# Kernel tuning notes

Hardware: AMD Instinct MI355X
Metric: run time of the kernel (lower is better)

## Reference

```python
import jax, jax.numpy as jnp
import numpy as np

K = 8
EPS = 1e-8


def setup_inputs() -> dict:
    key = jax.random.key(0)
    tokens = jax.random.normal(key, (32, 1024, 256), dtype=jnp.float32)
    return {"tokens": tokens}


def reference(tokens) -> jnp.ndarray:
    # tokens: [B, N, D] -> adjacency [B, N, N] float32 (0/1), mutual kNN, no self-loops
    B, N, D = tokens.shape
    tn = tokens / (jnp.linalg.norm(tokens, axis=-1, keepdims=True) + EPS)
    sim = jnp.einsum('bnd,bmd->bnm', tn, tn)  # [B, N, N] cosine similarity
    # mask diagonal (add_self=False)
    diag = jnp.eye(N, dtype=bool)
    sim = jnp.where(diag[None, :, :], -jnp.inf, sim)
    k = min(K, N - 1)
    _, topk_idx = jax.lax.top_k(sim, k)  # [B, N, k]
    b_idx = jnp.arange(B)[:, None, None]
    r_idx = jnp.arange(N)[None, :, None]
    adj = jnp.zeros((B, N, N), dtype=bool).at[b_idx, r_idx, topk_idx].set(True)
    # mutual kNN: keep edge only if both directions selected
    adj = adj & jnp.swapaxes(adj, 1, 2)
    return adj.astype(jnp.float32)
```

## Files before the change

### kernel.cpp

```cpp
#include <hip/hip_runtime.h>
#include <math.h>
#include <stdint.h>

#define B_ 32
#define N_ 1024
#define D_ 256
#define K_ 8
#define CAND 12

typedef unsigned short u16;
typedef unsigned int u32;
typedef __attribute__((ext_vector_type(8))) short s16x8;
typedef __attribute__((ext_vector_type(16))) float f32x16;

__device__ inline void cp16(const void* g, void* l) {
    __builtin_amdgcn_global_load_lds((const __attribute__((address_space(1))) void*)g,
                                     (__attribute__((address_space(3))) void*)l, 16, 0, 0);
}

__device__ inline u16 f2bf(float f) {
    uint32_t u = __float_as_uint(f);
    return (u16)((u + 0x7fffu + ((u >> 16) & 1u)) >> 16);
}
__device__ inline u32 umax32(u32 a, u32 b) { return a > b ? a : b; }
__device__ inline u32 umin32(u32 a, u32 b) { return a < b ? a : b; }

__global__ __launch_bounds__(256) void prep_kernel(const float* __restrict__ tok,
                                                   double* __restrict__ invn,
                                                   u16* __restrict__ xhi) {
    const int tid = threadIdx.x;
    const int wave = tid >> 6, lane = tid & 63;
    const int row = blockIdx.x * 4 + wave;
    const float4 v = *reinterpret_cast<const float4*>(tok + (size_t)row * D_ + lane * 4);
    double s = (double)v.x * v.x + (double)v.y * v.y +
               (double)v.z * v.z + (double)v.w * v.w;
    #pragma unroll
    for (int off = 32; off > 0; off >>= 1) s += __shfl_xor(s, off, 64);
    const double inv = 1.0 / (sqrt(s) + 1e-8);
    if (lane == 0) invn[row] = inv;
    ushort4 h;
    h.x = f2bf((float)(v.x * inv));
    h.y = f2bf((float)(v.y * inv));
    h.z = f2bf((float)(v.z * inv));
    h.w = f2bf((float)(v.w * inv));
    *reinterpret_cast<ushort4*>(xhi + (size_t)row * D_ + lane * 4) = h;
}

__global__ __launch_bounds__(256, 4) void sim_topk_kernel(const u16* __restrict__ Xhi,
                                                          u32* __restrict__ candk,
                                                          int* __restrict__ candj) {
    __shared__ __align__(16) char smem[16384];
    char* tiles = smem;
    u32*  keysL = (u32*)smem;

    const int id    = blockIdx.x;
    const int chunk = id >> 3;
    const int b   = (id & 7) * 4 + (chunk >> 5);
    const int rem = chunk & 31;
    const int i0  = (rem >> 1) * 64;
    const int jh  = rem & 1;

    const int tid = threadIdx.x;
    const int w = tid >> 6, lane = tid & 63;
    const int mq = w >> 1, nq = w & 1;
    const int half = lane >> 5;
    const int il = lane & 31;

    const u16* XhiB = Xhi + (size_t)b * N_ * D_;

    const int srr = lane >> 3, spp = lane & 7;
    const int sgoff = (spp ^ srr) * 8;
    const int srow  = w * 16 + srr;

    const int ra = mq * 32 + il;
    const int rb = nq * 32 + il;
    const int xa = ra & 7, xb = rb & 7;

    s16x8 Ahf[4][4];
    #pragma unroll
    for (int kc = 0; kc < 4; ++kc) {
        __syncthreads();
        #pragma unroll
        for (int t = 0; t < 2; ++t) {
            const int rr = srow + t * 8;
            cp16(XhiB + (size_t)(i0 + rr) * D_ + kc * 64 + sgoff,
                 tiles + w * 2048 + t * 1024);
        }
        __syncthreads();
        #pragma unroll
        for (int ks = 0; ks < 4; ++ks) {
            const int ca = ((ks * 2 + half) ^ xa) * 16;
            Ahf[kc][ks] = *(const s16x8*)(tiles + ra * 128 + ca);
        }
    }
    __syncthreads();

    auto STAGE_B = [&](int round, int bufn) {
        const int j0n = (jh * 8 + (round >> 2)) * 64;
        const int kcn = round & 3;
        char* bdst = tiles + bufn * 8192 + w * 2048;
        #pragma unroll
        for (int t = 0; t < 2; ++t) {
            const int rr = srow + t * 8;
            cp16(XhiB + (size_t)(j0n + rr) * D_ + kcn * 64 + sgoff, bdst + t * 1024);
        }
    };

    const int diag_jt = i0 >> 6;
    u32 keys[CAND];
    #pragma unroll
    for (int c = 0; c < CAND; ++c) keys[c] = 0u;

    STAGE_B(0, 0);

    for (int lt = 0; lt < 8; ++lt) {
        const int jt = jh * 8 + lt;
        f32x16 acc;
        #pragma unroll
        for (int c = 0; c < 16; ++c) acc[c] = 0.0f;

        #pragma unroll
        for (int kc = 0; kc < 4; ++kc) {
            const int r = lt * 4 + kc;
            const int cur = r & 1;
            if (r < 31) {
                STAGE_B(r + 1, cur ^ 1);
                asm volatile("s_waitcnt vmcnt(2)" ::: "memory");
            } else {
                asm volatile("s_waitcnt vmcnt(0)" ::: "memory");
            }
            __builtin_amdgcn_s_barrier();
            __builtin_amdgcn_sched_barrier(0);
            const char* bb = tiles + cur * 8192;
            #pragma unroll
            for (int ks = 0; ks < 4; ++ks) {
                const int cb = ((ks * 2 + half) ^ xb) * 16;
                const s16x8 bh = *(const s16x8*)(bb + rb * 128 + cb);
                acc = __builtin_amdgcn_mfma_f32_32x32x16_bf16(bh, Ahf[kc][ks], acc, 0, 0, 0);
            }
            __builtin_amdgcn_sched_barrier(0);
            __builtin_amdgcn_s_barrier();
        }

        const u32 codebase = (u32)(jt << 4);
        const bool diag = (jt == diag_jt) && (mq == nq);
        #pragma unroll
        for (int rg = 0; rg < 16; ++rg) {
            const u32 u = __float_as_uint(acc[rg]);
            const u32 mono = u ^ ((u32)(((int)u) >> 31) | 0x80000000u);
            u32 key = (mono & 0xFFFFFF00u) | (codebase + (u32)rg);
            if (diag && ((rg & 3) + 8 * (rg >> 2) + 4 * half == il)) key = 0u;
            u32 t = key;
            #pragma unroll
            for (int c = 0; c < CAND; ++c) {
                const u32 hi = umax32(keys[c], t);
                t = umin32(keys[c], t);
                keys[c] = hi;
            }
        }
    }

    __syncthreads();
    {
        const int r = mq * 32 + il;
        const int s = nq * 2 + half;
        u32* dst = keysL + (r * 4 + s) * CAND;
        #pragma unroll
        for (int c = 0; c < CAND; ++c) dst[c] = keys[c];
    }
    __syncthreads();

    if (tid < 64) {
        const u32* kl = keysL + tid * (4 * CAND);
        const size_t base = ((size_t)(b * N_ + i0 + tid) * 2 + jh) * CAND;
        int p0 = 0, p1 = 0, p2 = 0, p3 = 0;
        #pragma unroll
        for (int o = 0; o < CAND; ++o) {
            const u32 k0v = kl[p0];
            const u32 k1v = kl[CAND + p1];
            const u32 k2v = kl[2 * CAND + p2];
            const u32 k3v = kl[3 * CAND + p3];
            int bg = 0; u32 bv = k0v;
            if (k1v > bv) { bv = k1v; bg = 1; }
            if (k2v > bv) { bv = k2v; bg = 2; }
            if (k3v > bv) { bv = k3v; bg = 3; }
            const int code = (int)(bv & 0xFFu);
            const int jtv = code >> 4, rg = code & 15;
            candk[base + o] = bv;
            candj[base + o] = jtv * 64 + (bg >> 1) * 32 + (rg & 3) + 8 * (rg >> 2)
                              + 4 * (bg & 1);
            p0 += (bg == 0); p1 += (bg == 1); p2 += (bg == 2); p3 += (bg == 3);
        }
    }
}

__global__ __launch_bounds__(512) void merge_rescore_kernel(const u32* __restrict__ candk,
                                                            const int* __restrict__ candj,
                                                            const float* __restrict__ tok,
                                                            const double* __restrict__ invn,
                                                            int* __restrict__ topk) {
    __shared__ int    mj[32 * CAND];
    __shared__ double dv[32 * CAND];
    const int tid = threadIdx.x;

    const int id    = blockIdx.x;
    const int chunk = id >> 3;
    const int b     = (id & 7) * 4 + (chunk >> 5);
    const int i0    = (chunk & 31) * 32;
    const int R0    = b * N_ + i0;

    if (tid < 32) {
        const size_t base = (size_t)(R0 + tid) * 2 * CAND;
        int p0 = 0, p1 = 0;
        #pragma unroll
        for (int o = 0; o < CAND; ++o) {
            const u32 k0 = candk[base + p0];
            const u32 k1 = candk[base + CAND + p1];
            if (k0 >= k1) { mj[tid * CAND + o] = candj[base + p0];        ++p0; }
            else          { mj[tid * CAND + o] = candj[base + CAND + p1]; ++p1; }
        }
    }
    __syncthreads();

    {
        const int q = tid >> 2, ql = tid & 3;
        const int r = q >> 2;
        const float* qi = tok + (size_t)(R0 + r) * D_;
        const double di = invn[R0 + r];
        #pragma unroll 1
        for (int rr = 0; rr < 3; ++rr) {
            const int c = (q & 3) * 3 + rr;
            const int j = mj[r * CAND + c];
            const float* qj = tok + (size_t)(b * N_ + j) * D_;
            double s = 0.0;
            #pragma unroll 4
            for (int k = 0; k < 16; ++k) {
                const float4 x = *reinterpret_cast<const float4*>(qi + k * 16 + ql * 4);
                const float4 y = *reinterpret_cast<const float4*>(qj + k * 16 + ql * 4);
                s += (double)x.x * y.x + (double)x.y * y.y +
                     (double)x.z * y.z + (double)x.w * y.w;
            }
            s += __shfl_xor(s, 1, 64);
            s += __shfl_xor(s, 2, 64);
            if (ql == 0) dv[r * CAND + c] = s * di * invn[b * N_ + j];
        }
    }
    __syncthreads();

    if (tid < 32) {
        const int out_base = (R0 + tid) * K_;
        #pragma unroll 1
        for (int c = 0; c < CAND; ++c) {
            const double dc = dv[tid * CAND + c]; const int jc = mj[tid * CAND + c];
            int rank = 0;
            #pragma unroll 1
            for (int c2 = 0; c2 < CAND; ++c2) {
                if (c2 == c) continue;
                const double d2 = dv[tid * CAND + c2]; const int j2 = mj[tid * CAND + c2];
                if (d2 > dc || (d2 == dc && j2 < jc)) ++rank;
            }
            if (rank < K_) topk[out_base + rank] = jc;
        }
    }
}

__global__ __launch_bounds__(256) void mutual_kernel(const int* __restrict__ topk,
                                                     float* __restrict__ out) {
    const int gid = blockIdx.x * 256 + threadIdx.x;
    const int row = gid >> 3, s = gid & 7;
    const int j = topk[row * K_ + s];
    const int i = row & (N_ - 1);
    const int* tj = topk + ((row & ~(N_ - 1)) + j) * K_;
    bool m = false;
    #pragma unroll
    for (int u = 0; u < K_; ++u) m = m || (tj[u] == i);
    if (m) out[(size_t)row * N_ + j] = 1.0f;
}

extern "C" void kernel_launch(void* const* d_in, const int* in_sizes, int n_in,
                              void* d_out, int out_size, void* d_ws, size_t ws_size,
                              hipStream_t stream) {
    const float* tok = (const float*)d_in[0];
    float* out = (float*)d_out;
    double* invn = (double*)d_ws;
    int* topk = (int*)((char*)d_ws + (size_t)B_ * N_ * sizeof(double));
    u16* xhi = (u16*)d_out;
    u32* candk = (u32*)((char*)d_out + (size_t)32 * 1024 * 1024);
    int* candj = (int*)((char*)d_out + (size_t)35 * 1024 * 1024);

    prep_kernel<<<dim3(B_ * N_ / 4), 256, 0, stream>>>(tok, invn, xhi);
    sim_topk_kernel<<<dim3(1024), 256, 0, stream>>>(xhi, candk, candj);
    merge_rescore_kernel<<<dim3(B_ * N_ / 32), 512, 0, stream>>>(candk, candj, tok, invn, topk);
    hipMemsetAsync(d_out, 0, (size_t)out_size * sizeof(float), stream);
    mutual_kernel<<<dim3(B_ * N_ * K_ / 256), 256, 0, stream>>>(topk, out);
}
```

Before: 258.9 us.

## Give each wave private LDS tiles to drop block barriers in sim-topk loop

Each wave now stages its own 32-row A and B slices into a private 8 KB LDS region, double-buffered, so the block-wide s_barrier pairs around every k-step are removed and only per-wave waitcnts remain. The prefetch of the next B tile is issued after the LDS reads and before the MFMAs, with a two-deep lookahead, and the A preload is pipelined the same way. The cost is doubled shared memory (32 KB per block) and redundant global loads, since waves sharing the same rows each fetch them separately. The memset size expression is also rewritten to an explicit constant.

```diff
diff --git a/kernel.cpp b/kernel.cpp
--- a/kernel.cpp
+++ b/kernel.cpp
@@ -49,9 +49,8 @@
 __global__ __launch_bounds__(256, 4) void sim_topk_kernel(const u16* __restrict__ Xhi,
                                                           u32* __restrict__ candk,
                                                           int* __restrict__ candj) {
-    __shared__ __align__(16) char smem[16384];
-    char* tiles = smem;
-    u32*  keysL = (u32*)smem;
+    __shared__ __align__(16) char smem[32768];
+    u32* keysL = (u32*)smem;
 
     const int id    = blockIdx.x;
     const int chunk = id >> 3;
@@ -70,48 +69,49 @@
 
     const int srr = lane >> 3, spp = lane & 7;
     const int sgoff = (spp ^ srr) * 8;
-    const int srow  = w * 16 + srr;
-
-    const int ra = mq * 32 + il;
-    const int rb = nq * 32 + il;
-    const int xa = ra & 7, xb = rb & 7;
-
-    s16x8 Ahf[4][4];
-    #pragma unroll
-    for (int kc = 0; kc < 4; ++kc) {
-        __syncthreads();
-        #pragma unroll
-        for (int t = 0; t < 2; ++t) {
-            const int rr = srow + t * 8;
-            cp16(XhiB + (size_t)(i0 + rr) * D_ + kc * 64 + sgoff,
-                 tiles + w * 2048 + t * 1024);
-        }
-        __syncthreads();
-        #pragma unroll
-        for (int ks = 0; ks < 4; ++ks) {
-            const int ca = ((ks * 2 + half) ^ xa) * 16;
-            Ahf[kc][ks] = *(const s16x8*)(tiles + ra * 128 + ca);
-        }
-    }
-    __syncthreads();
-
+    char* const wbase = smem + w * 8192;
+
+    const int x7 = il & 7;
+    int loff[4];
+    #pragma unroll
+    for (int ks = 0; ks < 4; ++ks) loff[ks] = il * 128 + (((ks * 2 + half) ^ x7) * 16);
+
+    auto STAGE_A = [&](int kc, int bufn) {
+        #pragma unroll
+        for (int t = 0; t < 4; ++t)
+            cp16(XhiB + (size_t)(i0 + mq * 32 + t * 8 + srr) * D_ + kc * 64 + sgoff,
+                 wbase + bufn * 4096 + t * 1024);
+    };
     auto STAGE_B = [&](int round, int bufn) {
         const int j0n = (jh * 8 + (round >> 2)) * 64;
         const int kcn = round & 3;
-        char* bdst = tiles + bufn * 8192 + w * 2048;
-        #pragma unroll
-        for (int t = 0; t < 2; ++t) {
-            const int rr = srow + t * 8;
-            cp16(XhiB + (size_t)(j0n + rr) * D_ + kcn * 64 + sgoff, bdst + t * 1024);
-        }
+        #pragma unroll
+        for (int t = 0; t < 4; ++t)
+            cp16(XhiB + (size_t)(j0n + nq * 32 + t * 8 + srr) * D_ + kcn * 64 + sgoff,
+                 wbase + bufn * 4096 + t * 1024);
     };
+
+    s16x8 Ahf[4][4];
+    STAGE_A(0, 0);
+    STAGE_A(1, 1);
+    #pragma unroll
+    for (int kc = 0; kc < 4; ++kc) {
+        asm volatile("s_waitcnt vmcnt(4)" ::: "memory");
+        __builtin_amdgcn_sched_barrier(0);
+        const char* ab = wbase + (kc & 1) * 4096;
+        #pragma unroll
+        for (int ks = 0; ks < 4; ++ks)
+            Ahf[kc][ks] = *(const s16x8*)(ab + loff[ks]);
+        asm volatile("s_waitcnt lgkmcnt(0)" ::: "memory");
+        __builtin_amdgcn_sched_barrier(0);
+        if (kc < 2) STAGE_A(kc + 2, kc & 1);
+        else        STAGE_B(kc - 2, kc & 1);
+    }
 
     const int diag_jt = i0 >> 6;
     u32 keys[CAND];
     #pragma unroll
     for (int c = 0; c < CAND; ++c) keys[c] = 0u;
-
-    STAGE_B(0, 0);
 
     for (int lt = 0; lt < 8; ++lt) {
         const int jt = jh * 8 + lt;
@@ -122,24 +122,20 @@
         #pragma unroll
         for (int kc = 0; kc < 4; ++kc) {
             const int r = lt * 4 + kc;
-            const int cur = r & 1;
-            if (r < 31) {
-                STAGE_B(r + 1, cur ^ 1);
-                asm volatile("s_waitcnt vmcnt(2)" ::: "memory");
-            } else {
-                asm volatile("s_waitcnt vmcnt(0)" ::: "memory");
-            }
-            __builtin_amdgcn_s_barrier();
+            if (r < 31) asm volatile("s_waitcnt vmcnt(4)" ::: "memory");
+            else        asm volatile("s_waitcnt vmcnt(0)" ::: "memory");
             __builtin_amdgcn_sched_barrier(0);
-            const char* bb = tiles + cur * 8192;
+            const char* bb = wbase + (r & 1) * 4096;
+            s16x8 bh[4];
             #pragma unroll
-            for (int ks = 0; ks < 4; ++ks) {
-                const int cb = ((ks * 2 + half) ^ xb) * 16;
-                const s16x8 bh = *(const s16x8*)(bb + rb * 128 + cb);
-                acc = __builtin_amdgcn_mfma_f32_32x32x16_bf16(bh, Ahf[kc][ks], acc, 0, 0, 0);
-            }
+            for (int ks = 0; ks < 4; ++ks)
+                bh[ks] = *(const s16x8*)(bb + loff[ks]);
+            asm volatile("s_waitcnt lgkmcnt(0)" ::: "memory");
             __builtin_amdgcn_sched_barrier(0);
-            __builtin_amdgcn_s_barrier();
+            if (r + 2 < 32) STAGE_B(r + 2, r & 1);
+            #pragma unroll
+            for (int ks = 0; ks < 4; ++ks)
+                acc = __builtin_amdgcn_mfma_f32_32x32x16_bf16(bh[ks], Ahf[kc][ks], acc, 0, 0, 0);
         }
 
         const u32 codebase = (u32)(jt << 4);
@@ -291,6 +287,6 @@
     prep_kernel<<<dim3(B_ * N_ / 4), 256, 0, stream>>>(tok, invn, xhi);
     sim_topk_kernel<<<dim3(1024), 256, 0, stream>>>(xhi, candk, candj);
     merge_rescore_kernel<<<dim3(B_ * N_ / 32), 512, 0, stream>>>(candk, candj, tok, invn, topk);
-    hipMemsetAsync(d_out, 0, (size_t)out_size * sizeof(float), stream);
+    hipMemsetAsync(d_out, 0, (size_t)B_ * N_ * N_ * sizeof(float), stream);
     mutual_kernel<<<dim3(B_ * N_ * K_ / 256), 256, 0, stream>>>(topk, out);
 }
```

Measured after the change: 259.1 us. No clear change (+0.1%).
